# Kernel optimization log

Measured on AMD Instinct MI355X. Metric: run time of the kernel, lower is better.

Reference implementation:

```python
import jax, jax.numpy as jnp
import numpy as np

B, N, E, K = 4, 8192, 1024, 2048  # batch, points, emb_dims, pool nodes (N//4)
KNN = 20


def _conv(w, x):  # 1x1 Conv1d, no bias: w [O,C], x [B,C,N]
    return jnp.einsum('oc,bcn->bon', w, x)


def _bn(x, s, b):  # eval-mode BN folded to per-channel scale/bias, x [B,C,N]
    return x * s[None, :, None] + b[None, :, None]


def _sqdist(a, b):  # a [B,3,N], b [B,3,M] -> [B,N,M] squared distances
    return ((a * a).sum(1)[:, :, None] + (b * b).sum(1)[:, None, :]
            - 2.0 * jnp.einsum('bcn,bcm->bnm', a, b))


def _bgather(f, idx):  # f [B,C,N], idx [B,...] -> [B,C,...]
    return jax.vmap(lambda ff, ii: ff[:, ii])(f, idx)


def _pool(xyz, feat, pw, pb, k):
    Bq, C, _ = feat.shape
    proj = _conv(pw, feat) + pb[None, :, None]          # [B,8C,N]
    vec = proj.max(-1).reshape(Bq, C, 8)                # [B,C,8]
    scores = jax.nn.sigmoid(jnp.einsum('bcn,bce->bne', feat, vec))  # [B,N,8]
    v, i = jax.lax.top_k(scores.transpose(0, 2, 1), k // 8)         # [B,8,k//8]
    values = v.transpose(0, 2, 1).reshape(Bq, -1)       # [B,k] (torch reshape order)
    idx = i.transpose(0, 2, 1).reshape(Bq, -1)
    node_static = _bgather(xyz, idx)                    # [B,3,k]
    node_feature = _bgather(feat, idx) * values[:, None, :]
    node = node_static * values[:, None, :]
    return node, node_feature, node_static


def _aggregate(xyz, node, feat, k):
    d = _sqdist(xyz, node)                               # [B,N,M]
    _, idx = jax.lax.top_k(-d.transpose(0, 2, 1), k)     # [B,M,k] nearest inputs per node
    grouped = _bgather(feat, idx)                        # [B,C,M,k]
    return grouped.max(-1)                               # [B,C,M]


def _unpool(node_xyz, unknown_xyz, feat):
    d = _sqdist(unknown_xyz, node_xyz)                   # [B,N,M]
    negd, idx = jax.lax.top_k(-d, 3)                     # 3-NN along M
    w = jax.nn.softmax(-negd, axis=-1)                   # softmax over sq-dists (faithful)
    grouped = _bgather(feat, idx)                        # [B,C,N,3]
    return (w[:, None, :, :] * grouped).sum(-1)


def _forward(x, conv1_w, bn1_s, bn1_b, conv2_w, bn2_s, bn2_b,
             conv2m_w, bn2m_s, bn2m_b, pool_w, pool_b,
             conv3_w, bn3_s, bn3_b, conv4_w, bn4_s, bn4_b,
             conv5_w, bn5_s, bn5_b, conv6_w, bn6c_s, bn6c_b,
             conv7_w, bn7c_s, bn7c_b, conv8_w, bn8_s, bn8_b,
             conv9_w, bn9_s, bn9_b, conv10_w,
             lin1_w, bn6h_s, bn6h_b, lin2_w, lin2_b, bn7h_s, bn7h_b,
             lin3_w, lin3_b):
    relu = jax.nn.relu
    xyz = x
    x1 = relu(_bn(_conv(conv1_w, x), bn1_s, bn1_b))      # [B,64,N]
    x2 = relu(_bn(_conv(conv2_w, x1), bn2_s, bn2_b))     # [B,64,N]
    xt1_ = jnp.concatenate([x1, x2], 1)                  # [B,128,N]
    xt1 = relu(_bn(_conv(conv2m_w, xt1_), bn2m_s, bn2m_b))  # [B,E,N]
    node1, nf1, node1_static = _pool(xyz, xt1_, pool_w, pool_b, K)
    agg = _aggregate(xyz, node1, xt1_, KNN)              # [B,128,K]
    h = jnp.concatenate([nf1, agg], 1)                   # [B,256,K]
    x3 = relu(_bn(_conv(conv3_w, h), bn3_s, bn3_b))
    x4 = relu(_bn(_conv(conv4_w, x3), bn4_s, bn4_b))
    xt2 = relu(_bn(_conv(conv5_w, jnp.concatenate([x3, x4], 1)), bn5_s, bn5_b))
    vector = jnp.concatenate([xt1.max(-1), xt2.max(-1)], 1)  # [B,2E]
    c = relu((vector @ lin1_w.T) * bn6h_s + bn6h_b)
    c = relu((c @ lin2_w.T + lin2_b) * bn7h_s + bn7h_b)
    logits_cls = c @ lin3_w.T + lin3_b                   # [B,15]
    vrep = jnp.broadcast_to(vector[:, :, None], (vector.shape[0], vector.shape[1], x4.shape[-1]))
    s = relu(_bn(_conv(conv6_w, jnp.concatenate([vrep, x4], 1)), bn6c_s, bn6c_b))
    s = relu(_bn(_conv(conv7_w, jnp.concatenate([s, x3], 1)), bn7c_s, bn7c_b))
    s = _unpool(node1, xyz, s)                           # [B,128,N]
    s = relu(_bn(_conv(conv8_w, jnp.concatenate([s, x2], 1)), bn8_s, bn8_b))
    s = relu(_bn(_conv(conv9_w, jnp.concatenate([s, x1], 1)), bn9_s, bn9_b))
    logits_seg = _conv(conv10_w, s)                      # [B,2,N]
    return (logits_cls, logits_seg, node1, node1_static)


def setup_inputs() -> dict:
    key = jax.random.key(0)
    keys = iter(jax.random.split(key, 80))
    def w(shape, scale=0.05):
        return jax.random.normal(next(keys), shape, jnp.float32) * scale
    inp = {'x': jax.random.normal(next(keys), (B, 3, N), jnp.float32)}
    conv_shapes = {'conv1_w': (64, 3), 'conv2_w': (64, 64), 'conv2m_w': (E, 128),
                   'conv3_w': (256, 256), 'conv4_w': (256, 256), 'conv5_w': (E, 512),
                   'conv6_w': (128, 2 * E + 256), 'conv7_w': (128, 384),
                   'conv8_w': (128, 192), 'conv9_w': (128, 192), 'conv10_w': (2, 128)}
    for n, s in conv_shapes.items():
        inp[n] = w(s)
    for n, c in [('bn1', 64), ('bn2', 64), ('bn2m', E), ('bn3', 256), ('bn4', 256),
                 ('bn5', E), ('bn6c', 128), ('bn7c', 128), ('bn8', 128), ('bn9', 128),
                 ('bn6h', 512), ('bn7h', 256)]:
        inp[n + '_s'] = 1.0 + w((c,))
        inp[n + '_b'] = w((c,))
    inp['pool_w'] = w((E, 128)); inp['pool_b'] = w((E,))
    inp['lin1_w'] = w((512, 2 * E))
    inp['lin2_w'] = w((256, 512)); inp['lin2_b'] = w((256,))
    inp['lin3_w'] = w((15, 256)); inp['lin3_b'] = w((15,))
    return inp


def reference(x, conv1_w, bn1_s, bn1_b, conv2_w, bn2_s, bn2_b,
              conv2m_w, bn2m_s, bn2m_b, pool_w, pool_b,
              conv3_w, bn3_s, bn3_b, conv4_w, bn4_s, bn4_b,
              conv5_w, bn5_s, bn5_b, conv6_w, bn6c_s, bn6c_b,
              conv7_w, bn7c_s, bn7c_b, conv8_w, bn8_s, bn8_b,
              conv9_w, bn9_s, bn9_b, conv10_w,
              lin1_w, bn6h_s, bn6h_b, lin2_w, lin2_b, bn7h_s, bn7h_b,
              lin3_w, lin3_b):
    return _forward(x, conv1_w, bn1_s, bn1_b, conv2_w, bn2_s, bn2_b,
                    conv2m_w, bn2m_s, bn2m_b, pool_w, pool_b,
                    conv3_w, bn3_s, bn3_b, conv4_w, bn4_s, bn4_b,
                    conv5_w, bn5_s, bn5_b, conv6_w, bn6c_s, bn6c_b,
                    conv7_w, bn7c_s, bn7c_b, conv8_w, bn8_s, bn8_b,
                    conv9_w, bn9_s, bn9_b, conv10_w,
                    lin1_w, bn6h_s, bn6h_b, lin2_w, lin2_b, bn7h_s, bn7h_b,
                    lin3_w, lin3_b)
```

## Files before the change

### kernel.cpp

```cpp
#include <hip/hip_runtime.h>
#include <math.h>

#define NPTS 8192
#define MNODE 2048

#define WS_XT1  0L
#define WS_A    4194304L
#define WS_B    8388608L
#define WS_C    12582912L
#define WS_D    14680064L
#define WS_TOPV 18874368L
#define WS_TOPI 18882560L
#define WS_NODE 18890752L
#define WS_MAXP 18915328L
#define WS_VEC  18919424L
#define WS_C1   18927616L
#define WS_C2   18929664L
#define WS_B6   18930688L
#define WS_K20  18931200L
#define WS_K3I  19095040L
#define WS_K3W  19193344L

__global__ __launch_bounds__(256) void k_conv1(const float* __restrict__ x,
                                               const float* __restrict__ W,
                                               const float* __restrict__ sc,
                                               const float* __restrict__ bi,
                                               float* __restrict__ out) {
    int t = blockIdx.x * 256 + threadIdx.x;
    int n = t & 8191, o = (t >> 13) & 63, b = t >> 19;
    const float* xb = x + (long)b * 3 * NPTS;
    float a = W[o * 3 + 0] * xb[n] + W[o * 3 + 1] * xb[NPTS + n] + W[o * 3 + 2] * xb[2 * NPTS + n];
    a = fmaxf(a * sc[o] + bi[o], 0.f);
    out[((long)b * 128 + o) * NPTS + n] = a;
}

__global__ __launch_bounds__(256) void k_conv2(const float* __restrict__ in,
                                               const float* __restrict__ W,
                                               const float* __restrict__ sc,
                                               const float* __restrict__ bi,
                                               float* __restrict__ out) {
    int t = blockIdx.x * 256 + threadIdx.x;
    int n = t & 8191, o = (t >> 13) & 63, b = t >> 19;
    const float* ip = in + (long)b * 128 * NPTS + n;
    const float* wp = W + o * 64;
    float a = 0.f;
#pragma unroll 8
    for (int c = 0; c < 64; ++c) a = fmaf(wp[c], ip[(long)c * NPTS], a);
    out[((long)b * 128 + 64 + o) * NPTS + n] = fmaxf(a * sc[o] + bi[o], 0.f);
}

#define CMAX_FMA16()                                                        \
    {                                                                       \
        const float4* wp4 = reinterpret_cast<const float4*>(Wl + c16);      \
        _Pragma("unroll")                                                   \
        for (int g = 0; g < 4; ++g) {                                       \
            float4 w = wp4[g];                                              \
            acc[4 * g + 0].x = fmaf(w.x, v.x, acc[4 * g + 0].x);            \
            acc[4 * g + 0].y = fmaf(w.x, v.y, acc[4 * g + 0].y);            \
            acc[4 * g + 0].z = fmaf(w.x, v.z, acc[4 * g + 0].z);            \
            acc[4 * g + 0].w = fmaf(w.x, v.w, acc[4 * g + 0].w);            \
            acc[4 * g + 1].x = fmaf(w.y, v.x, acc[4 * g + 1].x);            \
            acc[4 * g + 1].y = fmaf(w.y, v.y, acc[4 * g + 1].y);            \
            acc[4 * g + 1].z = fmaf(w.y, v.z, acc[4 * g + 1].z);            \
            acc[4 * g + 1].w = fmaf(w.y, v.w, acc[4 * g + 1].w);            \
            acc[4 * g + 2].x = fmaf(w.z, v.x, acc[4 * g + 2].x);            \
            acc[4 * g + 2].y = fmaf(w.z, v.y, acc[4 * g + 2].y);            \
            acc[4 * g + 2].z = fmaf(w.z, v.z, acc[4 * g + 2].z);            \
            acc[4 * g + 2].w = fmaf(w.z, v.w, acc[4 * g + 2].w);            \
            acc[4 * g + 3].x = fmaf(w.w, v.x, acc[4 * g + 3].x);            \
            acc[4 * g + 3].y = fmaf(w.w, v.y, acc[4 * g + 3].y);            \
            acc[4 * g + 3].z = fmaf(w.w, v.z, acc[4 * g + 3].z);            \
            acc[4 * g + 3].w = fmaf(w.w, v.w, acc[4 * g + 3].w);            \
        }                                                                   \
    }

__global__ __launch_bounds__(256) void k_convmax(
        const float* __restrict__ in, int C, long ibs,
        const float* __restrict__ W1, const float* __restrict__ cb1,
        const float* __restrict__ sc1, const float* __restrict__ bi1, int relu1,
        float* __restrict__ pmax1,
        const float* __restrict__ W2, const float* __restrict__ cb2,
        const float* __restrict__ sc2, const float* __restrict__ bi2, int relu2,
        float* __restrict__ pmax2,
        int wpitch, int O, int Nn) {
    extern __shared__ float sm_[];
    float* Wl = sm_;
    float* red = sm_;
    int b = blockIdx.z;
    int ns = blockIdx.x;
    int oblocks = O >> 4;
    int setid = (int)blockIdx.y / oblocks;
    int og0 = ((int)blockIdx.y - setid * oblocks) * 16;
    const float* W  = setid ? W2 : W1;
    const float* cb = setid ? cb2 : cb1;
    const float* sc = setid ? sc2 : sc1;
    const float* bi = setid ? bi2 : bi1;
    int do_relu     = setid ? relu2 : relu1;
    float* pmax     = setid ? pmax2 : pmax1;
    for (int t = threadIdx.x; t < 16 * C; t += 256) {
        int c = t >> 4, o = t & 15;
        Wl[t] = W[(long)(og0 + o) * wpitch + c];
    }
    __syncthreads();
    int n0 = ns * 1024 + threadIdx.x * 4;
    float4 acc[16];
#pragma unroll
    for (int o = 0; o < 16; ++o) acc[o] = make_float4(0.f, 0.f, 0.f, 0.f);
    const float* p = in + (long)b * ibs + n0;
    float4 v = *reinterpret_cast<const float4*>(p);
    for (int c = 0; c < C - 1; ++c) {
        float4 vn = *reinterpret_cast<const float4*>(p + (long)(c + 1) * Nn);
        int c16 = c * 16;
        CMAX_FMA16();
        v = vn;
    }
    {
        int c16 = (C - 1) * 16;
        CMAX_FMA16();
    }
    float h2[16];
#pragma unroll
    for (int o = 0; o < 16; ++o) {
        float cbv = cb ? cb[og0 + o] : 0.f;
        float scv = sc ? sc[og0 + o] : 1.f;
        float biv = bi ? bi[og0 + o] : 0.f;
        float4 a = acc[o];
        float vx = (a.x + cbv) * scv + biv;
        float vy = (a.y + cbv) * scv + biv;
        float vz = (a.z + cbv) * scv + biv;
        float vw = (a.w + cbv) * scv + biv;
        if (do_relu) {
            vx = fmaxf(vx, 0.f); vy = fmaxf(vy, 0.f);
            vz = fmaxf(vz, 0.f); vw = fmaxf(vw, 0.f);
        }
        h2[o] = fmaxf(fmaxf(vx, vy), fmaxf(vz, vw));
    }
    __syncthreads();
#pragma unroll
    for (int o = 0; o < 16; ++o) red[o * 257 + threadIdx.x] = h2[o];
    __syncthreads();
    for (int ls = 7; ls >= 0; --ls) {
        int s = 1 << ls;
        for (int w = threadIdx.x; w < 16 * s; w += 256) {
            int o = w >> ls, i = w & (s - 1);
            float* r = red + o * 257;
            r[i] = fmaxf(r[i], r[i + s]);
        }
        __syncthreads();
    }
    if (threadIdx.x < 16)
        pmax[((long)ns * 4 + b) * O + og0 + threadIdx.x] = red[threadIdx.x * 257];
}

__global__ __launch_bounds__(256) void k_maxred2(const float* __restrict__ pA, int nsA, int OA,
                                                 float* __restrict__ outA, long obsA,
                                                 const float* __restrict__ pB, int nsB, int OB,
                                                 float* __restrict__ outB, long obsB,
                                                 int blocksA) {
    const float* pm; int ns, O; float* out; long obs; int bid = blockIdx.x;
    if (bid < blocksA) { pm = pA; ns = nsA; O = OA; out = outA; obs = obsA; }
    else { pm = pB; ns = nsB; O = OB; out = outB; obs = obsB; bid -= blocksA; }
    int t = bid * 256 + threadIdx.x;
    if (t >= 4 * O) return;
    int o = t % O, b = t / O;
    float m = -3.0e38f;
    for (int s = 0; s < ns; ++s) m = fmaxf(m, pm[((long)s * 4 + b) * O + o]);
    out[(long)b * obs + o] = m;
}

__global__ __launch_bounds__(256) void k_maxred(const float* __restrict__ pmax, int nsplit,
                                                int O, float* __restrict__ out, long obs) {
    int t = blockIdx.x * 256 + threadIdx.x;
    if (t >= 4 * O) return;
    int o = t % O, b = t / O;
    float m = -3.0e38f;
    for (int s = 0; s < nsplit; ++s) m = fmaxf(m, pmax[((long)s * 4 + b) * O + o]);
    out[(long)b * obs + o] = m;
}

#define CONV_FMA8()                                                         \
    {                                                                       \
        const float4* wp4 = reinterpret_cast<const float4*>(Wl + c8);       \
        _Pragma("unroll")                                                   \
        for (int g = 0; g < 2; ++g) {                                       \
            float4 w = wp4[g];                                              \
            acc[4 * g + 0].x = fmaf(w.x, v.x, acc[4 * g + 0].x);            \
            acc[4 * g + 0].y = fmaf(w.x, v.y, acc[4 * g + 0].y);            \
            acc[4 * g + 0].z = fmaf(w.x, v.z, acc[4 * g + 0].z);            \
            acc[4 * g + 0].w = fmaf(w.x, v.w, acc[4 * g + 0].w);            \
            acc[4 * g + 1].x = fmaf(w.y, v.x, acc[4 * g + 1].x);            \
            acc[4 * g + 1].y = fmaf(w.y, v.y, acc[4 * g + 1].y);            \
            acc[4 * g + 1].z = fmaf(w.y, v.z, acc[4 * g + 1].z);            \
            acc[4 * g + 1].w = fmaf(w.y, v.w, acc[4 * g + 1].w);            \
            acc[4 * g + 2].x = fmaf(w.z, v.x, acc[4 * g + 2].x);            \
            acc[4 * g + 2].y = fmaf(w.z, v.y, acc[4 * g + 2].y);            \
            acc[4 * g + 2].z = fmaf(w.z, v.z, acc[4 * g + 2].z);            \
            acc[4 * g + 2].w = fmaf(w.z, v.w, acc[4 * g + 2].w);            \
            acc[4 * g + 3].x = fmaf(w.w, v.x, acc[4 * g + 3].x);            \
            acc[4 * g + 3].y = fmaf(w.w, v.y, acc[4 * g + 3].y);            \
            acc[4 * g + 3].z = fmaf(w.w, v.z, acc[4 * g + 3].z);            \
            acc[4 * g + 3].w = fmaf(w.w, v.w, acc[4 * g + 3].w);            \
        }                                                                   \
    }

__global__ __launch_bounds__(256) void k_conv(const float* __restrict__ in1, int C1, long ibs1,
                                              const float* __restrict__ in2, int C2, long ibs2,
                                              const float* __restrict__ W, int wpitch,
                                              const float* __restrict__ extra,
                                              const float* __restrict__ sc,
                                              const float* __restrict__ bi, int do_relu,
                                              float* __restrict__ out, long obs, int O, int Nn) {
    __shared__ float Wl[384 * 8];
    int b = blockIdx.z;
    int og0 = blockIdx.y * 8;
    int on = O - og0; if (on > 8) on = 8;
    int Ct = C1 + C2;
    for (int t = threadIdx.x; t < Ct * 8; t += 256) {
        int c = t >> 3, o = t & 7;
        Wl[t] = (o < on) ? W[(long)(og0 + o) * wpitch + c] : 0.f;
    }
    __syncthreads();
    int n0 = blockIdx.x * 1024 + threadIdx.x * 4;
    float4 acc[8];
#pragma unroll
    for (int o = 0; o < 8; ++o) acc[o] = make_float4(0.f, 0.f, 0.f, 0.f);
    const float* p1 = in1 + (long)b * ibs1 + n0;
    {
        float4 v = *reinterpret_cast<const float4*>(p1);
        for (int c = 0; c < C1 - 1; ++c) {
            float4 vn = *reinterpret_cast<const float4*>(p1 + (long)(c + 1) * Nn);
            int c8 = c * 8;
            CONV_FMA8();
            v = vn;
        }
        int c8 = (C1 - 1) * 8;
        CONV_FMA8();
    }
    if (in2) {
        const float* p2 = in2 + (long)b * ibs2 + n0;
        float4 v = *reinterpret_cast<const float4*>(p2);
        for (int c = 0; c < C2 - 1; ++c) {
            float4 vn = *reinterpret_cast<const float4*>(p2 + (long)(c + 1) * Nn);
            int c8 = (C1 + c) * 8;
            CONV_FMA8();
            v = vn;
        }
        int c8 = (Ct - 1) * 8;
        CONV_FMA8();
    }
#pragma unroll
    for (int o = 0; o < 8; ++o) {
        if (o < on) {
            float e = extra ? extra[(long)b * O + og0 + o] : 0.f;
            float s = sc ? sc[og0 + o] : 1.f;
            float bv = bi ? bi[og0 + o] : 0.f;
            float4 a = acc[o];
            a.x = (a.x + e) * s + bv;
            a.y = (a.y + e) * s + bv;
            a.z = (a.z + e) * s + bv;
            a.w = (a.w + e) * s + bv;
            if (do_relu) {
                a.x = fmaxf(a.x, 0.f); a.y = fmaxf(a.y, 0.f);
                a.z = fmaxf(a.z, 0.f); a.w = fmaxf(a.w, 0.f);
            }
            *reinterpret_cast<float4*>(out + (long)b * obs + (long)(og0 + o) * Nn + n0) = a;
        }
    }
}

__global__ __launch_bounds__(256) void k_scores(const float* __restrict__ feat,
                                                const float* __restrict__ maxp,
                                                float* __restrict__ scores) {
    __shared__ float vl[1024];
    int b = blockIdx.z;
    for (int t = threadIdx.x; t < 1024; t += 256) vl[t] = maxp[b * 1024 + t];
    __syncthreads();
    int n0 = blockIdx.x * 1024 + threadIdx.x * 4;
    float4 acc[8];
#pragma unroll
    for (int e = 0; e < 8; ++e) acc[e] = make_float4(0.f, 0.f, 0.f, 0.f);
    const float* p = feat + (long)b * 128 * NPTS + n0;
    for (int c = 0; c < 128; ++c) {
        float4 v = *reinterpret_cast<const float4*>(p + (long)c * NPTS);
#pragma unroll
        for (int e = 0; e < 8; ++e) {
            float w = vl[c * 8 + e];
            acc[e].x = fmaf(w, v.x, acc[e].x);
            acc[e].y = fmaf(w, v.y, acc[e].y);
            acc[e].z = fmaf(w, v.z, acc[e].z);
            acc[e].w = fmaf(w, v.w, acc[e].w);
        }
    }
#pragma unroll
    for (int e = 0; e < 8; ++e) {
        float4 a = acc[e];
        a.x = 1.f / (1.f + expf(-a.x));
        a.y = 1.f / (1.f + expf(-a.y));
        a.z = 1.f / (1.f + expf(-a.z));
        a.w = 1.f / (1.f + expf(-a.w));
        *reinterpret_cast<float4*>(scores + ((long)b * 8 + e) * NPTS + n0) = a;
    }
}

__global__ __launch_bounds__(256) void k_sorta(const float* __restrict__ scores,
                                               unsigned int* __restrict__ kout,
                                               unsigned short* __restrict__ iout) {
    __shared__ unsigned int kv[1024];
    __shared__ unsigned short ki[1024];
    int ch = blockIdx.x & 7;
    const float* sp = scores + (long)(blockIdx.x >> 3) * NPTS + ch * 1024;
    for (int t = threadIdx.x; t < 1024; t += 256) {
        kv[t] = __float_as_uint(sp[t]) ^ 0xFFFFFFFFu;
        ki[t] = (unsigned short)(ch * 1024 + t);
    }
    __syncthreads();
    for (int k = 2; k <= 1024; k <<= 1) {
        for (int j = k >> 1; j > 0; j >>= 1) {
            for (int t = threadIdx.x; t < 1024; t += 256) {
                int ixj = t ^ j;
                if (ixj > t) {
                    unsigned int va = kv[t], vb = kv[ixj];
                    unsigned short ia = ki[t], ib = ki[ixj];
                    bool up = ((t & k) == 0);
                    bool gt = (va > vb) || (va == vb && ia > ib);
                    if (gt == up) { kv[t] = vb; kv[ixj] = va; ki[t] = ib; ki[ixj] = ia; }
                }
            }
            __syncthreads();
        }
    }
    if (threadIdx.x < 256) {
        kout[blockIdx.x * 256 + threadIdx.x] = kv[threadIdx.x];
        iout[blockIdx.x * 256 + threadIdx.x] = ki[threadIdx.x];
    }
}

__global__ __launch_bounds__(512) void k_sortb(const unsigned int* __restrict__ kin,
                                               const unsigned short* __restrict__ iin,
                                               float* __restrict__ topv,
                                               int* __restrict__ topi) {
    __shared__ unsigned int kv[2048];
    __shared__ unsigned short ki[2048];
    int be = blockIdx.x, b = be >> 3, e = be & 7;
    for (int t = threadIdx.x; t < 2048; t += 512) {
        kv[t] = kin[be * 2048 + t];
        ki[t] = iin[be * 2048 + t];
    }
    __syncthreads();
    for (int k = 2; k <= 2048; k <<= 1) {
        for (int j = k >> 1; j > 0; j >>= 1) {
            for (int t = threadIdx.x; t < 2048; t += 512) {
                int ixj = t ^ j;
                if (ixj > t) {
                    unsigned int va = kv[t], vb = kv[ixj];
                    unsigned short ia = ki[t], ib = ki[ixj];
                    bool up = ((t & k) == 0);
                    bool gt = (va > vb) || (va == vb && ia > ib);
                    if (gt == up) { kv[t] = vb; kv[ixj] = va; ki[t] = ib; ki[ixj] = ia; }
                }
            }
            __syncthreads();
        }
    }
    for (int r = threadIdx.x; r < 256; r += 512) {
        int j = r * 8 + e;
        topv[b * 2048 + j] = __uint_as_float(kv[r] ^ 0xFFFFFFFFu);
        topi[b * 2048 + j] = (int)ki[r];
    }
}

__global__ __launch_bounds__(256) void k_poolgather(const float* __restrict__ xyz,
                                                    const float* __restrict__ topv,
                                                    const int* __restrict__ topi,
                                                    float* __restrict__ node_ws,
                                                    float* __restrict__ out_node,
                                                    float* __restrict__ out_nstat) {
    int t = blockIdx.x * 256 + threadIdx.x;
    int j = t & 2047, b = t >> 11;
    int i = topi[b * 2048 + j];
    float v = topv[b * 2048 + j];
#pragma unroll
    for (int k = 0; k < 3; ++k) {
        float sx = xyz[((long)b * 3 + k) * NPTS + i];
        float nd = sx * v;
        out_nstat[((long)b * 3 + k) * MNODE + j] = sx;
        out_node[((long)b * 3 + k) * MNODE + j] = nd;
        node_ws[((long)b * 3 + k) * MNODE + j] = nd;
    }
}

__global__ __launch_bounds__(256) void k_nf1(const float* __restrict__ feat,
                                             const float* __restrict__ topv,
                                             const int* __restrict__ topi,
                                             float* __restrict__ h) {
    int t = blockIdx.x * 256 + threadIdx.x;
    int j = t & 2047, c = (t >> 11) & 127, b = t >> 18;
    int i = topi[b * 2048 + j];
    float v = topv[b * 2048 + j];
    h[((long)b * 256 + c) * MNODE + j] = feat[((long)b * 128 + c) * NPTS + i] * v;
}

__device__ __forceinline__ unsigned int fsortbits(float f) {
    unsigned int u = __float_as_uint(f);
    return u ^ ((unsigned int)((int)u >> 31) | 0x80000000u);
}

__global__ __launch_bounds__(256) void k_knn20(const float* __restrict__ xyz,
                                               const float* __restrict__ node,
                                               int* __restrict__ k20) {
    __shared__ unsigned int s1[256];
    __shared__ int s2[256];
    __shared__ int lcnt;
    int m = blockIdx.x & 2047, b = blockIdx.x >> 11;
    int t = threadIdx.x;
    float nx = node[((long)b * 3 + 0) * MNODE + m];
    float ny = node[((long)b * 3 + 1) * MNODE + m];
    float nz = node[((long)b * 3 + 2) * MNODE + m];
    float sm = nx * nx + ny * ny + nz * nz;
    const float* xb = xyz + (long)b * 3 * NPTS;
    unsigned int kmin = 0xFFFFFFFFu;
    for (int i = 0; i < 32; ++i) {
        int n = i * 256 + t;
        float px = xb[n], py = xb[NPTS + n], pz = xb[2 * NPTS + n];
        float d = (px * px + py * py + pz * pz) + sm - 2.f * (px * nx + py * ny + pz * nz);
        unsigned int key = fsortbits(d);
        kmin = key < kmin ? key : kmin;
    }
    s1[t] = kmin;
    if (t == 0) lcnt = 0;
    __syncthreads();
    for (int k = 2; k <= 256; k <<= 1) {
        for (int j = k >> 1; j > 0; j >>= 1) {
            int ixj = t ^ j;
            if (ixj > t) {
                unsigned int va = s1[t], vb = s1[ixj];
                bool up = ((t & k) == 0);
                if ((va > vb) == up) { s1[t] = vb; s1[ixj] = va; }
            }
            __syncthreads();
        }
    }
    unsigned int keyT = s1[19];
    __syncthreads();
    for (int i = 0; i < 32; ++i) {
        int n = i * 256 + t;
        float px = xb[n], py = xb[NPTS + n], pz = xb[2 * NPTS + n];
        float d = (px * px + py * py + pz * pz) + sm - 2.f * (px * nx + py * ny + pz * nz);
        unsigned int key = fsortbits(d);
        if (key <= keyT) {
            int p = atomicAdd(&lcnt, 1);
            if (p < 128) { s1[p] = key; s2[p] = n; }
        }
    }
    __syncthreads();
    int cnt = lcnt;
    if (cnt <= 128) {
        if (t >= cnt && t < 128) { s1[t] = 0xFFFFFFFFu; s2[t] = 0x7FFFFFFF; }
        __syncthreads();
        for (int k = 2; k <= 128; k <<= 1) {
            for (int j = k >> 1; j > 0; j >>= 1) {
                if (t < 128) {
                    int ixj = t ^ j;
                    if (ixj > t) {
                        unsigned int va = s1[t], vb = s1[ixj];
                        int ia = s2[t], ib = s2[ixj];
                        bool up = ((t & k) == 0);
                        bool gt = (va > vb) || (va == vb && ia > ib);
                        if (gt == up) { s1[t] = vb; s1[ixj] = va; s2[t] = ib; s2[ixj] = ia; }
                    }
                }
                __syncthreads();
            }
        }
        if (t < 20) k20[((long)b * 2048 + m) * 20 + t] = s2[t];
    } else {
        unsigned int lastk = 0u; int lasti = -1;
        for (int r = 0; r < 20; ++r) {
            unsigned int bk = 0xFFFFFFFFu; int bi = 0x7FFFFFFF;
            for (int i = 0; i < 32; ++i) {
                int n = i * 256 + t;
                float px = xb[n], py = xb[NPTS + n], pz = xb[2 * NPTS + n];
                float d = (px * px + py * py + pz * pz) + sm - 2.f * (px * nx + py * ny + pz * nz);
                unsigned int key = fsortbits(d);
                bool gtlast = (key > lastk) || (key == lastk && n > lasti);
                bool ltbest = (key < bk) || (key == bk && n < bi);
                if (gtlast && ltbest) { bk = key; bi = n; }
            }
            s1[t] = bk; s2[t] = bi;
            __syncthreads();
            for (int s = 128; s > 0; s >>= 1) {
                if (t < s) {
                    unsigned int vo = s1[t + s]; int io = s2[t + s];
                    unsigned int vm = s1[t]; int im = s2[t];
                    if (vo < vm || (vo == vm && io < im)) { s1[t] = vo; s2[t] = io; }
                }
                __syncthreads();
            }
            if (t == 0) k20[((long)b * 2048 + m) * 20 + r] = s2[0];
            lastk = s1[0]; lasti = s2[0];
            __syncthreads();
        }
    }
}

__global__ __launch_bounds__(256) void k_agg(const float* __restrict__ feat,
                                             const int* __restrict__ k20,
                                             float* __restrict__ h) {
    int t = blockIdx.x * 256 + threadIdx.x;
    int m = t & 2047, c = (t >> 11) & 127, b = t >> 18;
    const int* ip = k20 + ((long)b * 2048 + m) * 20;
    const float* fb = feat + ((long)b * 128 + c) * NPTS;
    float mx = -3.0e38f;
#pragma unroll
    for (int q = 0; q < 20; ++q) mx = fmaxf(mx, fb[ip[q] & 8191]);
    h[((long)b * 256 + 128 + c) * MNODE + m] = mx;
}

__global__ __launch_bounds__(256) void k_gemv(const float* __restrict__ in, int C,
                                              const float* __restrict__ W, int wpitch,
                                              const float* __restrict__ lb,
                                              const float* __restrict__ sc,
                                              const float* __restrict__ bi, int do_relu,
                                              float* __restrict__ out, int O) {
    __shared__ float red[256];
    int o = blockIdx.x;
    int t = threadIdx.x;
    const float* wp = W + (long)o * wpitch;
    float a0 = 0.f, a1 = 0.f, a2 = 0.f, a3 = 0.f;
    for (int c = t * 4; c < C; c += 1024) {
        float4 w = *reinterpret_cast<const float4*>(wp + c);
        float4 v0 = *reinterpret_cast<const float4*>(in + 0L * C + c);
        float4 v1 = *reinterpret_cast<const float4*>(in + 1L * C + c);
        float4 v2 = *reinterpret_cast<const float4*>(in + 2L * C + c);
        float4 v3 = *reinterpret_cast<const float4*>(in + 3L * C + c);
        a0 += w.x * v0.x + w.y * v0.y + w.z * v0.z + w.w * v0.w;
        a1 += w.x * v1.x + w.y * v1.y + w.z * v1.z + w.w * v1.w;
        a2 += w.x * v2.x + w.y * v2.y + w.z * v2.z + w.w * v2.w;
        a3 += w.x * v3.x + w.y * v3.y + w.z * v3.z + w.w * v3.w;
    }
    float lbv = lb ? lb[o] : 0.f;
    float scv = sc ? sc[o] : 1.f;
    float biv = bi ? bi[o] : 0.f;
#pragma unroll
    for (int b = 0; b < 4; ++b) {
        float a = (b == 0) ? a0 : (b == 1) ? a1 : (b == 2) ? a2 : a3;
        __syncthreads();
        red[t] = a;
        __syncthreads();
        for (int s2 = 128; s2 > 0; s2 >>= 1) {
            if (t < s2) red[t] += red[t + s2];
            __syncthreads();
        }
        if (t == 0) {
            float r = (red[0] + lbv) * scv + biv;
            if (do_relu) r = fmaxf(r, 0.f);
            out[(long)b * O + o] = r;
        }
    }
}

__global__ __launch_bounds__(256) void k_knn3(const float* __restrict__ xyz,
                                              const float* __restrict__ node,
                                              int* __restrict__ k3i, float* __restrict__ k3w) {
    __shared__ float sx[2048], sy[2048], sz[2048], sn[2048];
    __shared__ float md[256][3];
    __shared__ int   mi[256][3];
    int b = blockIdx.x >> 8;
    int pbase = (blockIdx.x & 255) * 32;
    int t = threadIdx.x;
    const float* nb = node + (long)b * 3 * MNODE;
    for (int j = t; j < 2048; j += 256) {
        float qx = nb[j], qy = nb[MNODE + j], qz = nb[2 * MNODE + j];
        sx[j] = qx; sy[j] = qy; sz[j] = qz;
        sn[j] = qx * qx + qy * qy + qz * qz;
    }
    __syncthreads();
    int i = t & 31, q = t >> 5;
    int n = pbase + i;
    float px = xyz[((long)b * 3 + 0) * NPTS + n];
    float py = xyz[((long)b * 3 + 1) * NPTS + n];
    float pz = xyz[((long)b * 3 + 2) * NPTS + n];
    float sp = px * px + py * py + pz * pz;
    float d0 = 3.0e38f, d1 = 3.0e38f, d2 = 3.0e38f;
    int i0 = 0, i1 = 0, i2 = 0;
    int m0 = q * 256;
#pragma unroll 4
    for (int k = 0; k < 256; ++k) {
        int m = m0 + k;
        float d = (sp + sn[m]) - 2.f * (px * sx[m] + py * sy[m] + pz * sz[m]);
        if (d < d2) {
            d2 = d; i2 = m;
            if (d2 < d1) { float td = d1; d1 = d2; d2 = td; int ti = i1; i1 = i2; i2 = ti; }
            if (d1 < d0) { float td = d0; d0 = d1; d1 = td; int ti = i0; i0 = i1; i1 = ti; }
        }
    }
    md[t][0] = d0; md[t][1] = d1; md[t][2] = d2;
    mi[t][0] = i0; mi[t][1] = i1; mi[t][2] = i2;
    __syncthreads();
    if (t < 32) {
        int p0 = 0, p1 = 0, p2 = 0, p3 = 0, p4 = 0, p5 = 0, p6 = 0, p7 = 0;
        float rd[3]; int ri[3];
#pragma unroll
        for (int r = 0; r < 3; ++r) {
            float bestd = 3.0e38f; int besti = 0x7FFFFFFF; int bestq = -1;
#define KNN3_HEAD(QQ, PV)                                                              \
            {                                                                          \
                float dd = md[(QQ) * 32 + t][PV]; int ii = mi[(QQ) * 32 + t][PV];      \
                if (dd < bestd || (dd == bestd && ii < besti)) {                       \
                    bestd = dd; besti = ii; bestq = (QQ);                              \
                }                                                                      \
            }
            KNN3_HEAD(0, p0) KNN3_HEAD(1, p1) KNN3_HEAD(2, p2) KNN3_HEAD(3, p3)
            KNN3_HEAD(4, p4) KNN3_HEAD(5, p5) KNN3_HEAD(6, p6) KNN3_HEAD(7, p7)
#undef KNN3_HEAD
            rd[r] = bestd; ri[r] = besti;
            p0 += (bestq == 0); p1 += (bestq == 1); p2 += (bestq == 2); p3 += (bestq == 3);
            p4 += (bestq == 4); p5 += (bestq == 5); p6 += (bestq == 6); p7 += (bestq == 7);
        }
        float mxd = fmaxf(rd[0], fmaxf(rd[1], rd[2]));
        float e0 = expf(rd[0] - mxd), e1 = expf(rd[1] - mxd), e2 = expf(rd[2] - mxd);
        float inv = 1.f / (e0 + e1 + e2);
        long base = ((long)b * NPTS + pbase + t) * 3;
        k3i[base] = ri[0]; k3i[base + 1] = ri[1]; k3i[base + 2] = ri[2];
        k3w[base] = e0 * inv; k3w[base + 1] = e1 * inv; k3w[base + 2] = e2 * inv;
    }
}

__global__ __launch_bounds__(256) void k_unpool(const float* __restrict__ s7,
                                                const int* __restrict__ k3i,
                                                const float* __restrict__ k3w,
                                                float* __restrict__ sup) {
    int t = blockIdx.x * 256 + threadIdx.x;
    int n = t & 8191, c = (t >> 13) & 127, b = t >> 20;
    long base = ((long)b * NPTS + n) * 3;
    const float* spp = s7 + ((long)b * 128 + c) * MNODE;
    float a = k3w[base] * spp[k3i[base]] + k3w[base + 1] * spp[k3i[base + 1]] +
              k3w[base + 2] * spp[k3i[base + 2]];
    sup[((long)b * 128 + c) * NPTS + n] = a;
}

extern "C" void kernel_launch(void* const* d_in, const int* in_sizes, int n_in,
                              void* d_out, int out_size, void* d_ws, size_t ws_size,
                              hipStream_t stream) {
    const float* x     = (const float*)d_in[0];
    const float* c1w   = (const float*)d_in[1];
    const float* c2w   = (const float*)d_in[2];
    const float* c2mw  = (const float*)d_in[3];
    const float* c3w   = (const float*)d_in[4];
    const float* c4w   = (const float*)d_in[5];
    const float* c5w   = (const float*)d_in[6];
    const float* c6w   = (const float*)d_in[7];
    const float* c7w   = (const float*)d_in[8];
    const float* c8w   = (const float*)d_in[9];
    const float* c9w   = (const float*)d_in[10];
    const float* c10w  = (const float*)d_in[11];
    const float* bn1s  = (const float*)d_in[12]; const float* bn1b  = (const float*)d_in[13];
    const float* bn2s  = (const float*)d_in[14]; const float* bn2b  = (const float*)d_in[15];
    const float* bn2ms = (const float*)d_in[16]; const float* bn2mb = (const float*)d_in[17];
    const float* bn3s  = (const float*)d_in[18]; const float* bn3b  = (const float*)d_in[19];
    const float* bn4s  = (const float*)d_in[20]; const float* bn4b  = (const float*)d_in[21];
    const float* bn5s  = (const float*)d_in[22]; const float* bn5b  = (const float*)d_in[23];
    const float* bn6cs = (const float*)d_in[24]; const float* bn6cb = (const float*)d_in[25];
    const float* bn7cs = (const float*)d_in[26]; const float* bn7cb = (const float*)d_in[27];
    const float* bn8s  = (const float*)d_in[28]; const float* bn8b  = (const float*)d_in[29];
    const float* bn9s  = (const float*)d_in[30]; const float* bn9b  = (const float*)d_in[31];
    const float* bn6hs = (const float*)d_in[32]; const float* bn6hb = (const float*)d_in[33];
    const float* bn7hs = (const float*)d_in[34]; const float* bn7hb = (const float*)d_in[35];
    const float* poolw = (const float*)d_in[36]; const float* poolb = (const float*)d_in[37];
    const float* l1w   = (const float*)d_in[38];
    const float* l2w   = (const float*)d_in[39]; const float* l2b   = (const float*)d_in[40];
    const float* l3w   = (const float*)d_in[41]; const float* l3b   = (const float*)d_in[42];

    float* ws   = (float*)d_ws;
    float* xt1  = ws + WS_XT1;
    float* x34  = ws + WS_A;
    float* scor = ws + WS_B;
    float* s8   = ws + WS_B;
    float* hbuf = ws + WS_C;
    float* s6   = ws + WS_C;
    float* s7   = ws + WS_C + 1048576L;
    float* sup  = ws + WS_D;
    float* s9   = ws + WS_D;
    float* topv = ws + WS_TOPV;
    int*   topi = (int*)(ws + WS_TOPI);
    float* node = ws + WS_NODE;
    float* maxp = ws + WS_MAXP;
    float* vec  = ws + WS_VEC;
    float* c1b  = ws + WS_C1;
    float* c2b_ = ws + WS_C2;
    float* b6   = ws + WS_B6;
    int*   k20  = (int*)(ws + WS_K20);
    float* pmax1 = ws + WS_K20;
    float* pmax2 = ws + WS_K20 + 32768;
    int*   k3i  = (int*)(ws + WS_K3I);
    float* k3w  = ws + WS_K3W;
    unsigned int*   sskeys = (unsigned int*)(ws + WS_A);
    unsigned short* ssidx  = (unsigned short*)(ws + WS_A + 65536);

    float* out       = (float*)d_out;
    float* out_cls   = out;
    float* out_seg   = out + 60;
    float* out_node  = out + 60 + 65536;
    float* out_nstat = out_node + 24576;

    k_conv1<<<dim3(8192), dim3(256), 0, stream>>>(x, c1w, bn1s, bn1b, xt1);
    k_conv2<<<dim3(8192), dim3(256), 0, stream>>>(xt1, c2w, bn2s, bn2b, xt1);
    k_convmax<<<dim3(8, 128, 4), dim3(256), 16 * 257 * 4, stream>>>(
        xt1, 128, 128L * NPTS,
        c2mw, nullptr, bn2ms, bn2mb, 1, pmax1,
        poolw, poolb, nullptr, nullptr, 0, pmax2,
        128, 1024, NPTS);
    k_maxred2<<<dim3(32), dim3(256), 0, stream>>>(pmax1, 8, 1024, vec, 2048,
                                                  pmax2, 8, 1024, maxp, 1024, 16);
    k_scores<<<dim3(8, 1, 4), dim3(256), 0, stream>>>(xt1, maxp, scor);
    k_sorta<<<dim3(256), dim3(256), 0, stream>>>(scor, sskeys, ssidx);
    k_sortb<<<dim3(32), dim3(512), 0, stream>>>(sskeys, ssidx, topv, topi);
    k_poolgather<<<dim3(32), dim3(256), 0, stream>>>(x, topv, topi, node, out_node, out_nstat);
    k_nf1<<<dim3(4096), dim3(256), 0, stream>>>(xt1, topv, topi, hbuf);
    k_knn20<<<dim3(8192), dim3(256), 0, stream>>>(x, node, k20);
    k_agg<<<dim3(4096), dim3(256), 0, stream>>>(xt1, k20, hbuf);
    k_conv<<<dim3(2, 32, 4), dim3(256), 0, stream>>>(hbuf, 256, 256L * MNODE, nullptr, 0, 0,
                                                     c3w, 256, nullptr, bn3s, bn3b, 1,
                                                     x34, 512L * MNODE, 256, MNODE);
    k_conv<<<dim3(2, 32, 4), dim3(256), 0, stream>>>(x34, 256, 512L * MNODE, nullptr, 0, 0,
                                                     c4w, 256, nullptr, bn4s, bn4b, 1,
                                                     x34 + 256L * MNODE, 512L * MNODE, 256, MNODE);
    k_convmax<<<dim3(2, 64, 4), dim3(256), 16 * 512 * 4, stream>>>(
        x34, 512, 512L * MNODE,
        c5w, nullptr, bn5s, bn5b, 1, pmax1,
        nullptr, nullptr, nullptr, nullptr, 0, nullptr,
        512, 1024, MNODE);
    k_maxred<<<dim3(16), dim3(256), 0, stream>>>(pmax1, 2, 1024, vec + 1024, 2048);
    k_gemv<<<dim3(512), dim3(256), 0, stream>>>(vec, 2048, l1w, 2048, nullptr, bn6hs, bn6hb, 1, c1b, 512);
    k_gemv<<<dim3(256), dim3(256), 0, stream>>>(c1b, 512, l2w, 512, l2b, bn7hs, bn7hb, 1, c2b_, 256);
    k_gemv<<<dim3(15), dim3(256), 0, stream>>>(c2b_, 256, l3w, 256, l3b, nullptr, nullptr, 0, out_cls, 15);
    k_gemv<<<dim3(128), dim3(256), 0, stream>>>(vec, 2048, c6w, 2304, nullptr, nullptr, nullptr, 0, b6, 128);
    k_conv<<<dim3(2, 16, 4), dim3(256), 0, stream>>>(x34 + 256L * MNODE, 256, 512L * MNODE,
                                                     nullptr, 0, 0, c6w + 2048, 2304, b6,
                                                     bn6cs, bn6cb, 1, s6, 128L * MNODE, 128, MNODE);
    k_conv<<<dim3(2, 16, 4), dim3(256), 0, stream>>>(s6, 128, 128L * MNODE, x34, 256, 512L * MNODE,
                                                     c7w, 384, nullptr, bn7cs, bn7cb, 1,
                                                     s7, 128L * MNODE, 128, MNODE);
    k_knn3<<<dim3(1024), dim3(256), 0, stream>>>(x, node, k3i, k3w);
    k_unpool<<<dim3(16384), dim3(256), 0, stream>>>(s7, k3i, k3w, sup);
    k_conv<<<dim3(8, 16, 4), dim3(256), 0, stream>>>(sup, 128, 128L * NPTS, xt1 + 64L * NPTS, 64,
                                                     128L * NPTS, c8w, 192, nullptr, bn8s, bn8b, 1,
                                                     s8, 128L * NPTS, 128, NPTS);
    k_conv<<<dim3(8, 16, 4), dim3(256), 0, stream>>>(s8, 128, 128L * NPTS, xt1, 64, 128L * NPTS,
                                                     c9w, 192, nullptr, bn9s, bn9b, 1,
                                                     s9, 128L * NPTS, 128, NPTS);
    k_conv<<<dim3(8, 1, 4), dim3(256), 0, stream>>>(s9, 128, 128L * NPTS, nullptr, 0, 0,
                                                    c10w, 128, nullptr, nullptr, nullptr, 0,
                                                    out_seg, 2L * NPTS, 2, NPTS);
    (void)in_sizes; (void)n_in; (void)out_size; (void)ws_size;
}
```

Measured before the change: 1.003 ms.

## Move conv-max GEMMs to bf16 MFMA with packed transposed operands

Adds packing kernels that convert activations (transposed to point-major) and weights into bf16 in an MFMA-friendly k-interleaved order. A new conv+BN+ReLU+max kernel runs the contraction with 16x16x32 bf16 MFMA instructions. It replaces the FP32 path for the conv2m max stage and the conv5 global max. The pool projection keeps its FP32 kernel, now launched with half the grid. The aim is to cut the FP32 FMA cost of the large 1024-output convolutions, at the price of extra pack passes and bf16 rounding error in the max-pooled features.

Result: faster. 941.7 us (-6.1%).

```diff
diff --git a/kernel.cpp b/kernel.cpp
--- a/kernel.cpp
+++ b/kernel.cpp
@@ -1,5 +1,9 @@
 #include <hip/hip_runtime.h>
 #include <math.h>
+
+typedef unsigned short u16;
+typedef short bf8 __attribute__((ext_vector_type(8)));
+typedef float f4 __attribute__((ext_vector_type(4)));
 
 #define NPTS 8192
 #define MNODE 2048
@@ -21,6 +25,12 @@
 #define WS_K3I  19095040L
 #define WS_K3W  19193344L
 
+__device__ __forceinline__ u16 bf16rne(float f) {
+    unsigned u = __float_as_uint(f);
+    unsigned r = u + 0x7FFFu + ((u >> 16) & 1u);
+    return (u16)(r >> 16);
+}
+
 __global__ __launch_bounds__(256) void k_conv1(const float* __restrict__ x,
                                                const float* __restrict__ W,
                                                const float* __restrict__ sc,
@@ -47,6 +57,85 @@
 #pragma unroll 8
     for (int c = 0; c < 64; ++c) a = fmaf(wp[c], ip[(long)c * NPTS], a);
     out[((long)b * 128 + 64 + o) * NPTS + n] = fmaxf(a * sc[o] + bi[o], 0.f);
+}
+
+
+__global__ __launch_bounds__(256) void k_packw(const float* __restrict__ W, int wpitch,
+                                               int C, int O, u16* __restrict__ out) {
+    int t = blockIdx.x * 256 + threadIdx.x;
+    if (t >= O * C) return;
+    int o = t / C, p = t - o * C;
+    int blk = p >> 5, pj = p & 31;
+    int g = pj >> 3, j = pj & 7;
+    int k = (blk << 5) + g * 4 + (j & 3) + 16 * (j >> 2);
+    out[t] = bf16rne(W[(long)o * wpitch + k]);
+}
+
+__global__ __launch_bounds__(256) void k_packT(const float* __restrict__ in, int C, int Nn,
+                                               u16* __restrict__ out) {
+    __shared__ float tile[32][33];
+    int b = blockIdx.z;
+    int k0 = blockIdx.y * 32, n0 = blockIdx.x * 32;
+    int tx = threadIdx.x & 31, ty = threadIdx.x >> 5;
+    for (int r = 0; r < 32; r += 8)
+        tile[ty + r][tx] = in[((long)b * C + k0 + ty + r) * Nn + n0 + tx];
+    __syncthreads();
+    for (int r = 0; r < 32; r += 8) {
+        int n = n0 + ty + r;
+        int p = tx;
+        int g = p >> 3, j = p & 7;
+        int kin = g * 4 + (j & 3) + 16 * (j >> 2);
+        out[((long)b * Nn + n) * C + k0 + p] = bf16rne(tile[kin][ty + r]);
+    }
+}
+
+__global__ __launch_bounds__(256) void k_cvmx_bf(const u16* __restrict__ in,
+                                                 const u16* __restrict__ wpk, int C,
+                                                 const float* __restrict__ sc,
+                                                 const float* __restrict__ bi, int do_relu,
+                                                 float* __restrict__ pmax, int O, int Nn) {
+    __shared__ float red[4][16][17];
+    int b = blockIdx.z, nc = blockIdx.x;
+    int lane = threadIdx.x & 63, w = threadIdx.x >> 6;
+    int o0 = (blockIdx.y * 4 + w) * 16;
+    const u16* wp = wpk + (long)(o0 + (lane & 15)) * C + ((lane >> 4) << 3);
+    const u16* ip = in + ((long)b * Nn + nc * 256 + (lane & 15)) * C + ((lane >> 4) << 3);
+    long nstride = 16L * C;
+    f4 acc[16];
+#pragma unroll
+    for (int t = 0; t < 16; ++t) acc[t] = (f4)(0.f);
+    for (int kk = 0; kk < C; kk += 32) {
+        bf8 a = *(const bf8*)(wp + kk);
+#pragma unroll
+        for (int t = 0; t < 16; ++t) {
+            bf8 bb = *(const bf8*)(ip + t * nstride + kk);
+            acc[t] = __builtin_amdgcn_mfma_f32_16x16x32_bf16(a, bb, acc[t], 0, 0, 0);
+        }
+    }
+#pragma unroll
+    for (int j = 0; j < 4; ++j) {
+        int ol = (lane >> 4) * 4 + j;
+        int o = o0 + ol;
+        float scv = sc ? sc[o] : 1.f;
+        float biv = bi ? bi[o] : 0.f;
+        float mm = -3.0e38f;
+#pragma unroll
+        for (int t = 0; t < 16; ++t) {
+            float v = acc[t][j] * scv + biv;
+            if (do_relu) v = fmaxf(v, 0.f);
+            mm = fmaxf(mm, v);
+        }
+        red[w][ol][lane & 15] = mm;
+    }
+    __syncthreads();
+    if (threadIdx.x < 64) {
+        int ww = threadIdx.x >> 4, oo = threadIdx.x & 15;
+        float mm = red[ww][oo][0];
+#pragma unroll
+        for (int i = 1; i < 16; ++i) mm = fmaxf(mm, red[ww][oo][i]);
+        int og = (blockIdx.y * 4 + ww) * 16 + oo;
+        pmax[((long)nc * 4 + b) * O + og] = mm;
+    }
 }
 
 #define CMAX_FMA16()                                                        \
@@ -691,11 +780,15 @@
     float* b6   = ws + WS_B6;
     int*   k20  = (int*)(ws + WS_K20);
     float* pmax1 = ws + WS_K20;
-    float* pmax2 = ws + WS_K20 + 32768;
+    float* pmax2 = ws + WS_K20 + 131072;
     int*   k3i  = (int*)(ws + WS_K3I);
     float* k3w  = ws + WS_K3W;
     unsigned int*   sskeys = (unsigned int*)(ws + WS_A);
     unsigned short* ssidx  = (unsigned short*)(ws + WS_A + 65536);
+    u16* xtb   = (u16*)(ws + WS_C);
+    u16* c2mwb = (u16*)(ws + WS_D);
+    u16* x34b  = (u16*)(ws + WS_B);
+    u16* c5wb  = (u16*)(ws + WS_B + 2097152);
 
     float* out       = (float*)d_out;
     float* out_cls   = out;
@@ -705,12 +798,16 @@
 
     k_conv1<<<dim3(8192), dim3(256), 0, stream>>>(x, c1w, bn1s, bn1b, xt1);
     k_conv2<<<dim3(8192), dim3(256), 0, stream>>>(xt1, c2w, bn2s, bn2b, xt1);
-    k_convmax<<<dim3(8, 128, 4), dim3(256), 16 * 257 * 4, stream>>>(
+    k_packT<<<dim3(256, 4, 4), dim3(256), 0, stream>>>(xt1, 128, NPTS, xtb);
+    k_packw<<<dim3(512), dim3(256), 0, stream>>>(c2mw, 128, 128, 1024, c2mwb);
+    k_cvmx_bf<<<dim3(32, 16, 4), dim3(256), 0, stream>>>(xtb, c2mwb, 128,
+                                                         bn2ms, bn2mb, 1, pmax1, 1024, NPTS);
+    k_convmax<<<dim3(8, 64, 4), dim3(256), 16 * 257 * 4, stream>>>(
         xt1, 128, 128L * NPTS,
-        c2mw, nullptr, bn2ms, bn2mb, 1, pmax1,
         poolw, poolb, nullptr, nullptr, 0, pmax2,
+        nullptr, nullptr, nullptr, nullptr, 0, nullptr,
         128, 1024, NPTS);
-    k_maxred2<<<dim3(32), dim3(256), 0, stream>>>(pmax1, 8, 1024, vec, 2048,
+    k_maxred2<<<dim3(32), dim3(256), 0, stream>>>(pmax1, 32, 1024, vec, 2048,
                                                   pmax2, 8, 1024, maxp, 1024, 16);
     k_scores<<<dim3(8, 1, 4), dim3(256), 0, stream>>>(xt1, maxp, scor);
     k_sorta<<<dim3(256), dim3(256), 0, stream>>>(scor, sskeys, ssidx);
@@ -725,12 +822,11 @@
     k_conv<<<dim3(2, 32, 4), dim3(256), 0, stream>>>(x34, 256, 512L * MNODE, nullptr, 0, 0,
                                                      c4w, 256, nullptr, bn4s, bn4b, 1,
                                                      x34 + 256L * MNODE, 512L * MNODE, 256, MNODE);
-    k_convmax<<<dim3(2, 64, 4), dim3(256), 16 * 512 * 4, stream>>>(
-        x34, 512, 512L * MNODE,
-        c5w, nullptr, bn5s, bn5b, 1, pmax1,
-        nullptr, nullptr, nullptr, nullptr, 0, nullptr,
-        512, 1024, MNODE);
-    k_maxred<<<dim3(16), dim3(256), 0, stream>>>(pmax1, 2, 1024, vec + 1024, 2048);
+    k_packT<<<dim3(64, 16, 4), dim3(256), 0, stream>>>(x34, 512, MNODE, x34b);
+    k_packw<<<dim3(2048), dim3(256), 0, stream>>>(c5w, 512, 512, 1024, c5wb);
+    k_cvmx_bf<<<dim3(8, 16, 4), dim3(256), 0, stream>>>(x34b, c5wb, 512,
+                                                        bn5s, bn5b, 1, pmax1, 1024, MNODE);
+    k_maxred<<<dim3(16), dim3(256), 0, stream>>>(pmax1, 8, 1024, vec + 1024, 2048);
     k_gemv<<<dim3(512), dim3(256), 0, stream>>>(vec, 2048, l1w, 2048, nullptr, bn6hs, bn6hb, 1, c1b, 512);
     k_gemv<<<dim3(256), dim3(256), 0, stream>>>(c1b, 512, l2w, 512, l2b, bn7hs, bn7hb, 1, c2b_, 256);
     k_gemv<<<dim3(15), dim3(256), 0, stream>>>(c2b_, 256, l3w, 256, l3b, nullptr, nullptr, 0, out_cls, 15);
```
